# Kernel tuning notes

Measured on AMD Instinct MI355X. Metric: run time of the kernel, lower is better.

The kernel has to match this reference:

```python
import jax, jax.numpy as jnp
import numpy as np

B, S, H, NH, FF, L = 2, 2048, 768, 12, 3072, 2
DH = H // NH
EPS = 1e-12
NEG = -10000.0


def setup_inputs() -> dict:
    key = jax.random.key(0)
    ks = jax.random.split(key, 10)
    w = lambda k, shp: jax.random.normal(k, shp, dtype=jnp.float32) * 0.02
    return {
        'hidden_states': jax.random.normal(ks[0], (B, S, H), dtype=jnp.float32),
        'attention_mask': jnp.ones((B, S), jnp.float32),
        'bias_matrix': jax.random.normal(ks[1], (S, S), dtype=jnp.float32) * 0.1,
        'bias_coef': jnp.ones((), jnp.float32),
        'Wq': w(ks[2], (L, H, H)), 'bq': jnp.zeros((L, H), jnp.float32),
        'Wk': w(ks[3], (L, H, H)), 'bk': jnp.zeros((L, H), jnp.float32),
        'Wv': w(ks[4], (L, H, H)), 'bv': jnp.zeros((L, H), jnp.float32),
        'Wo': w(ks[5], (L, H, H)), 'bo': jnp.zeros((L, H), jnp.float32),
        'ln1_g': jnp.ones((L, H), jnp.float32), 'ln1_b': jnp.zeros((L, H), jnp.float32),
        'Wi': w(ks[6], (L, H, FF)), 'bi': jnp.zeros((L, FF), jnp.float32),
        'Wo2': w(ks[7], (L, FF, H)), 'bo2': jnp.zeros((L, H), jnp.float32),
        'ln2_g': jnp.ones((L, H), jnp.float32), 'ln2_b': jnp.zeros((L, H), jnp.float32),
    }


def _layer_norm(x, g, b):
    mu = jnp.mean(x, axis=-1, keepdims=True)
    var = jnp.mean(jnp.square(x - mu), axis=-1, keepdims=True)
    return (x - mu) * jax.lax.rsqrt(var + EPS) * g + b


def reference(hidden_states, attention_mask, bias_matrix, bias_coef,
              Wq, bq, Wk, bk, Wv, bv, Wo, bo, ln1_g, ln1_b,
              Wi, bi, Wo2, bo2, ln2_g, ln2_b):
    # extended additive mask: [B,1,1,S]
    ext_mask = (1.0 - attention_mask)[:, None, None, :] * NEG
    bias = bias_matrix[None, None] * bias_coef  # [1,1,S,S]
    x = hidden_states
    scale = 1.0 / np.sqrt(DH)
    for i in range(L):
        q = (x @ Wq[i] + bq[i]).reshape(B, S, NH, DH).transpose(0, 2, 1, 3)
        k = (x @ Wk[i] + bk[i]).reshape(B, S, NH, DH).transpose(0, 2, 1, 3)
        v = (x @ Wv[i] + bv[i]).reshape(B, S, NH, DH).transpose(0, 2, 1, 3)
        scores = jnp.einsum('bhqd,bhkd->bhqk', q, k) * scale
        scores = scores + bias + ext_mask
        probs = jax.nn.softmax(scores, axis=-1)  # dropout = identity (eval)
        ctx = jnp.einsum('bhqk,bhkd->bhqd', probs, v)
        ctx = ctx.transpose(0, 2, 1, 3).reshape(B, S, H)
        attn_out = ctx @ Wo[i] + bo[i]
        x = _layer_norm(attn_out + x, ln1_g[i], ln1_b[i])
        inter = jax.nn.gelu(x @ Wi[i] + bi[i], approximate=False)
        ffn_out = inter @ Wo2[i] + bo2[i]
        x = _layer_norm(ffn_out + x, ln2_g[i], ln2_b[i])
    return x
```

## Files before the change

kernel.cpp:

```cpp
#include <hip/hip_runtime.h>
#include <hip/hip_bf16.h>
#include <math.h>

#define BB     2
#define SS     2048
#define HH     768
#define NHEAD  12
#define DHEAD  64
#define FFD    3072
#define NLAYER 2
#define MTOK   (BB*SS)

typedef __attribute__((ext_vector_type(8))) short bf16x8;
typedef __attribute__((ext_vector_type(4))) short bf16x4;
typedef __attribute__((ext_vector_type(4))) float f32x4;

__device__ __forceinline__ short f2bs(float f) {
    union { float f; unsigned u; } v; v.f = f;
    unsigned r = v.u + 0x7FFF + ((v.u >> 16) & 1);
    return (short)(r >> 16);
}
__device__ __forceinline__ float bs2f(short s) {
    union { unsigned u; float f; } v; v.u = ((unsigned)(unsigned short)s) << 16;
    return v.f;
}
__device__ __forceinline__ void gl2lds16(const short* g, short* l) {
    __builtin_amdgcn_global_load_lds(
        (const __attribute__((address_space(1))) unsigned int*)g,
        (__attribute__((address_space(3))) unsigned int*)l, 16, 0, 0);
}

struct TJobs { const float* src[8]; short* dst[8]; };

__global__ __launch_bounds__(256)
void transpose_cvt_batch(TJobs jobs, int K, int N)
{
    const float* __restrict__ W  = jobs.src[blockIdx.z];
    short* __restrict__ Wt = jobs.dst[blockIdx.z];
    __shared__ short tile[32][33];
    const int k0 = blockIdx.x * 32, n0 = blockIdx.y * 32;
    const int tx = threadIdx.x & 31, ty = threadIdx.x >> 5;
#pragma unroll
    for (int i = 0; i < 4; i++)
        tile[ty + i*8][tx] = f2bs(W[(size_t)(k0 + ty + i*8) * N + n0 + tx]);
    __syncthreads();
#pragma unroll
    for (int i = 0; i < 4; i++)
        Wt[(size_t)(n0 + ty + i*8) * K + k0 + tx] = tile[tx][ty + i*8];
}

__global__ __launch_bounds__(256)
void cvt_bf16(const float* __restrict__ src, short* __restrict__ dst, int n)
{
    const int i = blockIdx.x * 256 + threadIdx.x;
    if (i < n) dst[i] = f2bs(src[i]);
}

__global__ __launch_bounds__(256)
void pack_bias(const float* __restrict__ bq, const float* __restrict__ bk,
               const float* __restrict__ bv, float* __restrict__ bqkv)
{
    const int t = blockIdx.x * 256 + threadIdx.x;
    if (t >= NLAYER * 2304) return;
    const int l = t / 2304, r = t % 2304;
    const float* src = (r < 768) ? bq : (r < 1536 ? bk : bv);
    bqkv[t] = src[l*768 + (r % 768)];
}

__global__ __launch_bounds__(256)
void bias_frag_prep(const float* __restrict__ biasM, const float* __restrict__ mask,
                    const float* __restrict__ coefp, short* __restrict__ bFrag)
{
    __shared__ float tile[64][129];
    const int tid = threadIdx.x;
    const int qb = blockIdx.x, q0 = qb*64, k0 = blockIdx.y*128;
#pragma unroll
    for (int p = 0; p < 8; p++) {
        const int row = p*8 + (tid >> 5);
        const int col = (tid & 31) * 4;
        float4 v = *(const float4*)&biasM[(size_t)(q0 + row)*SS + k0 + col];
        tile[row][col+0] = v.x; tile[row][col+1] = v.y;
        tile[row][col+2] = v.z; tile[row][col+3] = v.w;
    }
    __syncthreads();
    const float coef = coefp[0];
    const int lane = tid & 63, w = tid >> 6;
    const int l16 = lane & 15, g = lane >> 4;
    const int qrow = w*16 + l16;
#pragma unroll
    for (int b = 0; b < BB; b++) {
#pragma unroll
        for (int kt = 0; kt < 8; kt++) {
            bf16x4 o;
#pragma unroll
            for (int r = 0; r < 4; r++) {
                const int kk = kt*16 + g*4 + r;
                const float madd = (1.f - mask[b*SS + k0 + kk]) * (-10000.0f);
                o[r] = f2bs(tile[qrow][kk] * coef + madd);
            }
            const size_t idx = ((((size_t)b*32 + qb)*4 + w)*128 + (k0>>4) + kt)*256 + lane*4;
            *(bf16x4*)&bFrag[idx] = o;
        }
    }
}

__global__ __launch_bounds__(256)
void gemm_mfma(const short* __restrict__ A, const short* __restrict__ Bt,
               const float* __restrict__ bias, short* __restrict__ C, int ldc,
               int M, int N, int K, int gelu, short* __restrict__ VtOut, int vsplit)
{
    __shared__ short sA[2][128*32];
    __shared__ short sB[2][128*32];
    const int tid  = threadIdx.x;
    const int w    = tid >> 6;
    const int lane = tid & 63;
    const int l16  = lane & 15, g = lane >> 4;
    const int wm   = w & 1, wn = w >> 1;
    const size_t m0 = (size_t)blockIdx.y * 128, n0 = (size_t)blockIdx.x * 128;

    const int srow = lane >> 2;
    const int kc   = lane & 3;

    f32x4 acc[4][4];
#pragma unroll
    for (int i = 0; i < 4; i++)
#pragma unroll
        for (int j = 0; j < 4; j++) acc[i][j] = (f32x4){0.f,0.f,0.f,0.f};

    const short* gA0 = A  + (m0 + w*32 +      srow) * (size_t)K + kc*8;
    const short* gA1 = A  + (m0 + w*32 + 16 + srow) * (size_t)K + kc*8;
    const short* gB0 = Bt + (n0 + w*32 +      srow) * (size_t)K + kc*8;
    const short* gB1 = Bt + (n0 + w*32 + 16 + srow) * (size_t)K + kc*8;
    const int oA0 = (w*32     )*32, oA1 = (w*32 + 16)*32;

    for (int k0 = 0; k0 < K; k0 += 64) {
        gl2lds16(gA0 + k0,      &sA[0][oA0]);
        gl2lds16(gA1 + k0,      &sA[0][oA1]);
        gl2lds16(gB0 + k0,      &sB[0][oA0]);
        gl2lds16(gB1 + k0,      &sB[0][oA1]);
        gl2lds16(gA0 + k0 + 32, &sA[1][oA0]);
        gl2lds16(gA1 + k0 + 32, &sA[1][oA1]);
        gl2lds16(gB0 + k0 + 32, &sB[1][oA0]);
        gl2lds16(gB1 + k0 + 32, &sB[1][oA1]);
        __syncthreads();

#pragma unroll
        for (int s = 0; s < 2; s++) {
            bf16x8 af[4], bfr[4];
#pragma unroll
            for (int mt = 0; mt < 4; mt++)
                af[mt] = *(const bf16x8*)&sA[s][(wm*64 + mt*16 + l16)*32 + g*8];
#pragma unroll
            for (int nt = 0; nt < 4; nt++)
                bfr[nt] = *(const bf16x8*)&sB[s][(wn*64 + nt*16 + l16)*32 + g*8];
#pragma unroll
            for (int mt = 0; mt < 4; mt++)
#pragma unroll
                for (int nt = 0; nt < 4; nt++)
                    acc[mt][nt] = __builtin_amdgcn_mfma_f32_16x16x32_bf16(
                                      af[mt], bfr[nt], acc[mt][nt], 0, 0, 0);
        }
        __syncthreads();
    }

#pragma unroll
    for (int mt = 0; mt < 4; mt++) {
        const size_t row0 = m0 + wm*64 + mt*16 + g*4;
#pragma unroll
        for (int nt = 0; nt < 4; nt++) {
            const size_t col = n0 + wn*64 + nt*16 + l16;
            if ((int)col >= vsplit) {
                short4 t;
                t.x = f2bs(acc[mt][nt][0] + bias[col]);
                t.y = f2bs(acc[mt][nt][1] + bias[col]);
                t.z = f2bs(acc[mt][nt][2] + bias[col]);
                t.w = f2bs(acc[mt][nt][3] + bias[col]);
                *(short4*)&VtOut[(size_t)(col - vsplit)*MTOK + row0] = t;
            } else {
#pragma unroll
                for (int r = 0; r < 4; r++) {
                    float v = acc[mt][nt][r] + bias[col];
                    if (gelu) v = 0.5f * v * (1.f + erff(v * 0.70710678118f));
                    C[(row0 + r) * (size_t)ldc + col] = f2bs(v);
                }
            }
        }
    }
}

__global__ __launch_bounds__(256)
void gemm_mfma_n64(const short* __restrict__ A, const short* __restrict__ Bt,
                   const float* __restrict__ bias, short* __restrict__ C, int ldc,
                   int M, int N, int K, int gelu)
{
    __shared__ short sA[2][128*32];
    __shared__ short sB[2][64*32];
    const int tid  = threadIdx.x;
    const int w    = tid >> 6;
    const int lane = tid & 63;
    const int l16  = lane & 15, g = lane >> 4;
    const int wm   = w & 1, wn = w >> 1;
    const size_t m0 = (size_t)blockIdx.y * 128, n0 = (size_t)blockIdx.x * 64;

    const int srow = lane >> 2;
    const int kc   = lane & 3;

    f32x4 acc[4][2];
#pragma unroll
    for (int i = 0; i < 4; i++)
#pragma unroll
        for (int j = 0; j < 2; j++) acc[i][j] = (f32x4){0.f,0.f,0.f,0.f};

    const short* gA0 = A  + (m0 + w*32 +      srow) * (size_t)K + kc*8;
    const short* gA1 = A  + (m0 + w*32 + 16 + srow) * (size_t)K + kc*8;
    const short* gB0 = Bt + (n0 + w*16 +      srow) * (size_t)K + kc*8;
    const int oA0 = (w*32     )*32, oA1 = (w*32 + 16)*32, oB0 = (w*16)*32;

    for (int k0 = 0; k0 < K; k0 += 64) {
        gl2lds16(gA0 + k0,      &sA[0][oA0]);
        gl2lds16(gA1 + k0,      &sA[0][oA1]);
        gl2lds16(gB0 + k0,      &sB[0][oB0]);
        gl2lds16(gA0 + k0 + 32, &sA[1][oA0]);
        gl2lds16(gA1 + k0 + 32, &sA[1][oA1]);
        gl2lds16(gB0 + k0 + 32, &sB[1][oB0]);
        __syncthreads();

#pragma unroll
        for (int s = 0; s < 2; s++) {
            bf16x8 af[4], bfr[2];
#pragma unroll
            for (int mt = 0; mt < 4; mt++)
                af[mt] = *(const bf16x8*)&sA[s][(wm*64 + mt*16 + l16)*32 + g*8];
#pragma unroll
            for (int nt = 0; nt < 2; nt++)
                bfr[nt] = *(const bf16x8*)&sB[s][(wn*32 + nt*16 + l16)*32 + g*8];
#pragma unroll
            for (int mt = 0; mt < 4; mt++)
#pragma unroll
                for (int nt = 0; nt < 2; nt++)
                    acc[mt][nt] = __builtin_amdgcn_mfma_f32_16x16x32_bf16(
                                      af[mt], bfr[nt], acc[mt][nt], 0, 0, 0);
        }
        __syncthreads();
    }

#pragma unroll
    for (int mt = 0; mt < 4; mt++) {
        const size_t row0 = m0 + wm*64 + mt*16 + g*4;
#pragma unroll
        for (int nt = 0; nt < 2; nt++) {
            const size_t col = n0 + wn*32 + nt*16 + l16;
#pragma unroll
            for (int r = 0; r < 4; r++) {
                float v = acc[mt][nt][r] + bias[col];
                if (gelu) v = 0.5f * v * (1.f + erff(v * 0.70710678118f));
                C[(row0 + r) * (size_t)ldc + col] = f2bs(v);
            }
        }
    }
}

__global__ __launch_bounds__(256, 4)
void attn_fused(const short* __restrict__ QK, const short* __restrict__ Vt,
                const short* __restrict__ bFrag, short* __restrict__ CTX)
{
    __shared__ short sK[128*72];
    __shared__ short sV[64*136];

    const int qb  = blockIdx.x;
    const int q0  = qb * 64;
    const int h   = blockIdx.y;
    const int b   = blockIdx.z;
    const int tid = threadIdx.x;
    const int w   = tid >> 6;
    const int lane = tid & 63;
    const int l16 = lane & 15;
    const int g   = lane >> 4;
    const float scale = 0.125f;

    const short* qrow = QK + ((size_t)(b*SS) + q0 + w*16 + l16) * 1536 + h*64;
    bf16x8 bQ0 = *(const bf16x8*)(qrow + g*8);
    bf16x8 bQ1 = *(const bf16x8*)(qrow + 32 + g*8);

    f32x4 O[4];
#pragma unroll
    for (int d = 0; d < 4; d++) O[d] = (f32x4){0.f,0.f,0.f,0.f};
    float m_q = -1e30f, l_q = 0.f;

    const int krow = tid >> 3, kch = tid & 7;
    const int vrow = tid >> 4, vch = tid & 15;
    const short* Kg = QK + ((size_t)(b*SS) + krow)*1536 + 768 + h*64 + kch*8;
    const short* Vg = Vt + ((size_t)(h*64 + vrow))*MTOK + b*SS + vch*8;
    const short* bF = bFrag + ((((size_t)b*32 + qb)*4 + w)*128)*256 + lane*4;

    bf16x8 kreg[4], vreg[4];
#pragma unroll
    for (int p = 0; p < 4; p++) {
        kreg[p] = *(const bf16x8*)(Kg + (size_t)(p*32)*1536);
        vreg[p] = *(const bf16x8*)(Vg + (size_t)(p*16)*MTOK);
    }

    for (int k0 = 0; k0 < SS; k0 += 128) {
        const short* bFt = bF + ((size_t)(k0 >> 4))*256;
        bf16x4 bb[8];
#pragma unroll
        for (int t = 0; t < 8; t++)
            bb[t] = *(const bf16x4*)(bFt + (size_t)t*256);

#pragma unroll
        for (int p = 0; p < 4; p++) {
            *(bf16x8*)&sK[(p*32 + krow)*72 + kch*8]   = kreg[p];
            *(bf16x8*)&sV[(p*16 + vrow)*136 + vch*8]  = vreg[p];
        }
        __syncthreads();

        if (k0 + 128 < SS) {
#pragma unroll
            for (int p = 0; p < 4; p++) {
                kreg[p] = *(const bf16x8*)(Kg + (size_t)(k0 + 128 + p*32)*1536);
                vreg[p] = *(const bf16x8*)(Vg + (size_t)(p*16)*MTOK + k0 + 128);
            }
        }

        float S[8][4];
#pragma unroll
        for (int t = 0; t < 8; t++) {
            bf16x8 aK0 = *(const bf16x8*)&sK[(t*16 + l16)*72 + g*8];
            bf16x8 aK1 = *(const bf16x8*)&sK[(t*16 + l16)*72 + 32 + g*8];
            f32x4 c = (f32x4){0.f,0.f,0.f,0.f};
            c = __builtin_amdgcn_mfma_f32_16x16x32_bf16(aK0, bQ0, c, 0, 0, 0);
            c = __builtin_amdgcn_mfma_f32_16x16x32_bf16(aK1, bQ1, c, 0, 0, 0);
#pragma unroll
            for (int r = 0; r < 4; r++)
                S[t][r] = c[r]*scale + bs2f(bb[t][r]);
        }

        float tm[8];
#pragma unroll
        for (int t = 0; t < 8; t++)
            tm[t] = fmaxf(fmaxf(S[t][0], S[t][1]), fmaxf(S[t][2], S[t][3]));
        float mx = fmaxf(fmaxf(fmaxf(tm[0], tm[1]), fmaxf(tm[2], tm[3])),
                         fmaxf(fmaxf(tm[4], tm[5]), fmaxf(tm[6], tm[7])));
        mx = fmaxf(mx, __shfl_xor(mx, 16));
        mx = fmaxf(mx, __shfl_xor(mx, 32));
        const float mnew  = fmaxf(m_q, mx);
        const float alpha = __expf(m_q - mnew);
        float ts[8];
#pragma unroll
        for (int t = 0; t < 8; t++) {
            float p0 = __expf(S[t][0] - mnew);
            float p1 = __expf(S[t][1] - mnew);
            float p2 = __expf(S[t][2] - mnew);
            float p3 = __expf(S[t][3] - mnew);
            S[t][0] = p0; S[t][1] = p1; S[t][2] = p2; S[t][3] = p3;
            ts[t] = (p0 + p1) + (p2 + p3);
        }
        float rs = ((ts[0] + ts[1]) + (ts[2] + ts[3]))
                 + ((ts[4] + ts[5]) + (ts[6] + ts[7]));
        rs += __shfl_xor(rs, 16);
        rs += __shfl_xor(rs, 32);
        l_q = l_q * alpha + rs;
        m_q = mnew;

#pragma unroll
        for (int r = 0; r < 4; r++) {
            const float ar = __shfl(alpha, g*4 + r);
#pragma unroll
            for (int d = 0; d < 4; d++) O[d][r] *= ar;
        }

#define PVU(u)                                                                 \
        {                                                                      \
            unsigned pa, pb, pc, pe;                                           \
            asm("v_cvt_pk_bf16_f32 %0, %1, %2" : "=v"(pa)                      \
                : "v"(S[2*(u)][0]),   "v"(S[2*(u)][1]));                       \
            asm("v_cvt_pk_bf16_f32 %0, %1, %2" : "=v"(pb)                      \
                : "v"(S[2*(u)][2]),   "v"(S[2*(u)][3]));                       \
            asm("v_cvt_pk_bf16_f32 %0, %1, %2" : "=v"(pc)                      \
                : "v"(S[2*(u)+1][0]), "v"(S[2*(u)+1][1]));                     \
            asm("v_cvt_pk_bf16_f32 %0, %1, %2" : "=v"(pe)                      \
                : "v"(S[2*(u)+1][2]), "v"(S[2*(u)+1][3]));                     \
            asm("v_permlane32_swap_b32 %0, %1" : "+v"(pa), "+v"(pc));          \
            asm("v_permlane16_swap_b32 %0, %1" : "+v"(pa), "+v"(pc));          \
            asm("v_permlane32_swap_b32 %0, %1" : "+v"(pb), "+v"(pe));          \
            asm("v_permlane16_swap_b32 %0, %1" : "+v"(pb), "+v"(pe));          \
            union { unsigned uw[4]; bf16x8 v; } P_;                            \
            P_.uw[0] = pa; P_.uw[1] = pb; P_.uw[2] = pc; P_.uw[3] = pe;        \
            _Pragma("unroll")                                                  \
            for (int d = 0; d < 4; d++) {                                      \
                bf16x8 vv = *(const bf16x8*)&sV[(d*16 + l16)*136 + (u)*32 + g*8]; \
                O[d] = __builtin_amdgcn_mfma_f32_16x16x32_bf16(                \
                           P_.v, vv, O[d], 0, 0, 0);                           \
            }                                                                  \
        }
        PVU(0)
        PVU(1)
        PVU(2)
        PVU(3)
#undef PVU

        __syncthreads();
    }

    float linv[4];
#pragma unroll
    for (int r = 0; r < 4; r++)
        linv[r] = 1.f / __shfl(l_q, g*4 + r);
#pragma unroll
    for (int d = 0; d < 4; d++)
#pragma unroll
        for (int r = 0; r < 4; r++)
            CTX[((size_t)(b*SS) + q0 + w*16 + g*4 + r)*HH + h*64 + d*16 + l16]
                = f2bs(O[d][r] * linv[r]);
}

__global__ __launch_bounds__(256)
void add_ln(const short* __restrict__ A, const short* __restrict__ R,
            const float* __restrict__ g, const float* __restrict__ beta,
            short* __restrict__ Out, float* __restrict__ OutF)
{
    const int lane = threadIdx.x & 63;
    const int row  = blockIdx.x * 4 + (threadIdx.x >> 6);
    const size_t base = (size_t)row * HH;

    float v[12];
    float s = 0.f;
#pragma unroll
    for (int p = 0; p < 3; p++) {
        const int c = p*256 + lane*4;
        bf16x4 av = *(const bf16x4*)&A[base + c];
        bf16x4 rv = *(const bf16x4*)&R[base + c];
#pragma unroll
        for (int j = 0; j < 4; j++) {
            float x = bs2f(av[j]) + bs2f(rv[j]);
            v[p*4 + j] = x;
            s += x;
        }
    }
    s += __shfl_xor(s, 1);  s += __shfl_xor(s, 2);  s += __shfl_xor(s, 4);
    s += __shfl_xor(s, 8);  s += __shfl_xor(s, 16); s += __shfl_xor(s, 32);
    const float mu = s * (1.f / HH);

    float s2 = 0.f;
#pragma unroll
    for (int j = 0; j < 12; j++) { float d = v[j] - mu; s2 += d * d; }
    s2 += __shfl_xor(s2, 1);  s2 += __shfl_xor(s2, 2);  s2 += __shfl_xor(s2, 4);
    s2 += __shfl_xor(s2, 8);  s2 += __shfl_xor(s2, 16); s2 += __shfl_xor(s2, 32);
    const float rstd = rsqrtf(s2 * (1.f / HH) + 1e-12f);

#pragma unroll
    for (int p = 0; p < 3; p++) {
        const int c = p*256 + lane*4;
        float4 gv = *(const float4*)&g[c];
        float4 bv = *(const float4*)&beta[c];
        float o0 = (v[p*4+0] - mu) * rstd * gv.x + bv.x;
        float o1 = (v[p*4+1] - mu) * rstd * gv.y + bv.y;
        float o2 = (v[p*4+2] - mu) * rstd * gv.z + bv.z;
        float o3 = (v[p*4+3] - mu) * rstd * gv.w + bv.w;
        bf16x4 ov; ov[0] = f2bs(o0); ov[1] = f2bs(o1); ov[2] = f2bs(o2); ov[3] = f2bs(o3);
        *(bf16x4*)&Out[base + c] = ov;
        if (OutF) {
            float4 of; of.x = o0; of.y = o1; of.z = o2; of.w = o3;
            *(float4*)&OutF[base + c] = of;
        }
    }
}

extern "C" void kernel_launch(void* const* d_in, const int* in_sizes, int n_in,
                              void* d_out, int out_size, void* d_ws, size_t ws_size,
                              hipStream_t stream)
{
    const float* hs    = (const float*)d_in[0];
    const float* mask  = (const float*)d_in[1];
    const float* biasM = (const float*)d_in[2];
    const float* coef  = (const float*)d_in[3];
    const float* Wq    = (const float*)d_in[4];
    const float* bq    = (const float*)d_in[5];
    const float* Wk    = (const float*)d_in[6];
    const float* bk    = (const float*)d_in[7];
    const float* Wv    = (const float*)d_in[8];
    const float* bv    = (const float*)d_in[9];
    const float* Wo    = (const float*)d_in[10];
    const float* bo    = (const float*)d_in[11];
    const float* ln1g  = (const float*)d_in[12];
    const float* ln1b  = (const float*)d_in[13];
    const float* Wi    = (const float*)d_in[14];
    const float* bi    = (const float*)d_in[15];
    const float* Wo2   = (const float*)d_in[16];
    const float* bo2   = (const float*)d_in[17];
    const float* ln2g  = (const float*)d_in[18];
    const float* ln2b  = (const float*)d_in[19];

    const size_t sH   = (size_t)MTOK * HH;
    const size_t sQK  = (size_t)MTOK * 1536;
    const size_t sVt  = (size_t)HH * MTOK;
    const size_t WPL  = 7077888;
    short* wt    = (short*)d_ws;
    float* bqkv  = (float*)(wt + 2*WPL);
    short* bFrag = (short*)(bqkv + 2*2304);
    short* X     = bFrag + (size_t)2*SS*SS;
    short* X2    = X  + sH;
    short* QK    = X2 + sH;
    short* Vt    = QK + sQK;
    short* CTX   = Vt + sVt;
    short* TMP   = QK;
    short* INTER = QK;
    short* TMP2  = X;

    const dim3 blk(256);

    TJobs jH, jI, jO;
    for (int l = 0; l < NLAYER; l++) {
        short* wl = wt + (size_t)l * WPL;
        jH.src[l*4+0] = Wq + (size_t)l*HH*HH;  jH.dst[l*4+0] = wl;
        jH.src[l*4+1] = Wk + (size_t)l*HH*HH;  jH.dst[l*4+1] = wl + 768*768;
        jH.src[l*4+2] = Wv + (size_t)l*HH*HH;  jH.dst[l*4+2] = wl + 1536*768;
        jH.src[l*4+3] = Wo + (size_t)l*HH*HH;  jH.dst[l*4+3] = wl + 1769472;
        jI.src[l] = Wi  + (size_t)l*HH*FFD;    jI.dst[l] = wl + 2359296;
        jO.src[l] = Wo2 + (size_t)l*FFD*HH;    jO.dst[l] = wl + 4718592;
    }
    transpose_cvt_batch<<<dim3(24,24,8), blk, 0, stream>>>(jH, HH, HH);
    transpose_cvt_batch<<<dim3(24,96,2), blk, 0, stream>>>(jI, HH, FFD);
    transpose_cvt_batch<<<dim3(96,24,2), blk, 0, stream>>>(jO, FFD, HH);
    bias_frag_prep<<<dim3(SS/64, SS/128), blk, 0, stream>>>(biasM, mask, coef, bFrag);
    pack_bias<<<dim3((NLAYER*2304 + 255)/256), blk, 0, stream>>>(bq, bk, bv, bqkv);
    cvt_bf16<<<dim3((int)((sH + 255)/256)), blk, 0, stream>>>(hs, X, (int)sH);

    const dim3 gQKV(2304/128, MTOK/128);
    const dim3 gH64(HH/64,    MTOK/128);
    const dim3 gFF (FFD/128,  MTOK/128);
    const dim3 gA  (SS/64, NHEAD, BB);
    const dim3 gLN (MTOK/4);
    const int NOSPLIT = 1 << 30;

    for (int l = 0; l < NLAYER; l++) {
        short* wl = wt + (size_t)l * WPL;
        gemm_mfma<<<gQKV, blk, 0, stream>>>(X, wl, bqkv + l*2304, QK, 1536,
                                            MTOK, 2304, HH, 0, Vt, 1536);
        attn_fused<<<gA, blk, 0, stream>>>(QK, Vt, bFrag, CTX);
        gemm_mfma_n64<<<gH64, blk, 0, stream>>>(CTX, wl + 1769472, bo + l*HH, TMP, HH,
                                                MTOK, HH, HH, 0);
        add_ln<<<gLN, blk, 0, stream>>>(TMP, X, ln1g + l*HH, ln1b + l*HH, X2, nullptr);
        gemm_mfma<<<gFF, blk, 0, stream>>>(X2, wl + 2359296, bi + l*FFD, INTER, FFD,
                                           MTOK, FFD, HH, 1, nullptr, NOSPLIT);
        gemm_mfma_n64<<<gH64, blk, 0, stream>>>(INTER, wl + 4718592, bo2 + l*HH, TMP2, HH,
                                                MTOK, HH, FFD, 0);
        add_ln<<<gLN, blk, 0, stream>>>(TMP2, X2, ln2g + l*HH, ln2b + l*HH, X,
                                        (l == NLAYER-1) ? (float*)d_out : nullptr);
    }
}
```

Before: 573.5 us.

## Split-K the N=768 GEMMs with fp32 partials reduced in LayerNorm; fold softmax scale

The two N=768 output GEMMs now split K in half across gridDim.z and write fp32 partial sums. The add+LayerNorm kernel sums the two partials, adds the bias and the residual, which doubles the number of blocks for those under-filled GEMMs. Separately, the 1/sqrt(d)*log2e factor is folded into the Q projection epilogue and the additive bias tile is pre-scaled by log2e, so attention uses exp2f and drops a multiply per score. Attention launch bounds drop from 4 to 3 waves per SIMD. The cost is extra fp32 partial traffic (two 4096x768 fp32 buffers) written and read back per GEMM.

```diff
diff --git a/kernel.cpp b/kernel.cpp
--- a/kernel.cpp
+++ b/kernel.cpp
@@ -10,6 +10,8 @@
 #define FFD    3072
 #define NLAYER 2
 #define MTOK   (BB*SS)
+#define LOG2E  1.4426950408889634f
+#define QSCALE 0.18033688011112042f
 
 typedef __attribute__((ext_vector_type(8))) short bf16x8;
 typedef __attribute__((ext_vector_type(4))) short bf16x4;
@@ -96,7 +98,7 @@
             for (int r = 0; r < 4; r++) {
                 const int kk = kt*16 + g*4 + r;
                 const float madd = (1.f - mask[b*SS + k0 + kk]) * (-10000.0f);
-                o[r] = f2bs(tile[qrow][kk] * coef + madd);
+                o[r] = f2bs((tile[qrow][kk] * coef + madd) * LOG2E);
             }
             const size_t idx = ((((size_t)b*32 + qb)*4 + w)*128 + (k0>>4) + kt)*256 + lane*4;
             *(bf16x4*)&bFrag[idx] = o;
@@ -107,7 +109,8 @@
 __global__ __launch_bounds__(256)
 void gemm_mfma(const short* __restrict__ A, const short* __restrict__ Bt,
                const float* __restrict__ bias, short* __restrict__ C, int ldc,
-               int M, int N, int K, int gelu, short* __restrict__ VtOut, int vsplit)
+               int M, int N, int K, int gelu, short* __restrict__ VtOut, int vsplit,
+               float qscale, int qcols)
 {
     __shared__ short sA[2][128*32];
     __shared__ short sB[2][128*32];
@@ -180,6 +183,7 @@
 #pragma unroll
                 for (int r = 0; r < 4; r++) {
                     float v = acc[mt][nt][r] + bias[col];
+                    if ((int)col < qcols) v *= qscale;
                     if (gelu) v = 0.5f * v * (1.f + erff(v * 0.70710678118f));
                     C[(row0 + r) * (size_t)ldc + col] = f2bs(v);
                 }
@@ -189,10 +193,11 @@
 }
 
 __global__ __launch_bounds__(256)
-void gemm_mfma_n64(const short* __restrict__ A, const short* __restrict__ Bt,
-                   const float* __restrict__ bias, short* __restrict__ C, int ldc,
-                   int M, int N, int K, int gelu)
-{
+void gemm_n64_splitk(const short* __restrict__ A, const short* __restrict__ Bt,
+                     float* __restrict__ P, int K)
+{
+    const int K2 = K >> 1;
+    const int z  = blockIdx.z;
     __shared__ short sA[2][128*32];
     __shared__ short sB[2][64*32];
     const int tid  = threadIdx.x;
@@ -211,12 +216,12 @@
 #pragma unroll
         for (int j = 0; j < 2; j++) acc[i][j] = (f32x4){0.f,0.f,0.f,0.f};
 
-    const short* gA0 = A  + (m0 + w*32 +      srow) * (size_t)K + kc*8;
-    const short* gA1 = A  + (m0 + w*32 + 16 + srow) * (size_t)K + kc*8;
-    const short* gB0 = Bt + (n0 + w*16 +      srow) * (size_t)K + kc*8;
+    const short* gA0 = A  + (m0 + w*32 +      srow) * (size_t)K + z*K2 + kc*8;
+    const short* gA1 = A  + (m0 + w*32 + 16 + srow) * (size_t)K + z*K2 + kc*8;
+    const short* gB0 = Bt + (n0 + w*16 +      srow) * (size_t)K + z*K2 + kc*8;
     const int oA0 = (w*32     )*32, oA1 = (w*32 + 16)*32, oB0 = (w*16)*32;
 
-    for (int k0 = 0; k0 < K; k0 += 64) {
+    for (int k0 = 0; k0 < K2; k0 += 64) {
         gl2lds16(gA0 + k0,      &sA[0][oA0]);
         gl2lds16(gA1 + k0,      &sA[0][oA1]);
         gl2lds16(gB0 + k0,      &sB[0][oB0]);
@@ -244,6 +249,7 @@
         __syncthreads();
     }
 
+    float* Pz = P + (size_t)z * MTOK * HH;
 #pragma unroll
     for (int mt = 0; mt < 4; mt++) {
         const size_t row0 = m0 + wm*64 + mt*16 + g*4;
@@ -251,16 +257,13 @@
         for (int nt = 0; nt < 2; nt++) {
             const size_t col = n0 + wn*32 + nt*16 + l16;
 #pragma unroll
-            for (int r = 0; r < 4; r++) {
-                float v = acc[mt][nt][r] + bias[col];
-                if (gelu) v = 0.5f * v * (1.f + erff(v * 0.70710678118f));
-                C[(row0 + r) * (size_t)ldc + col] = f2bs(v);
-            }
-        }
-    }
-}
-
-__global__ __launch_bounds__(256, 4)
+            for (int r = 0; r < 4; r++)
+                Pz[(row0 + r) * (size_t)HH + col] = acc[mt][nt][r];
+        }
+    }
+}
+
+__global__ __launch_bounds__(256, 3)
 void attn_fused(const short* __restrict__ QK, const short* __restrict__ Vt,
                 const short* __restrict__ bFrag, short* __restrict__ CTX)
 {
@@ -276,7 +279,6 @@
     const int lane = tid & 63;
     const int l16 = lane & 15;
     const int g   = lane >> 4;
-    const float scale = 0.125f;
 
     const short* qrow = QK + ((size_t)(b*SS) + q0 + w*16 + l16) * 1536 + h*64;
     bf16x8 bQ0 = *(const bf16x8*)(qrow + g*8);
@@ -332,7 +334,7 @@
             c = __builtin_amdgcn_mfma_f32_16x16x32_bf16(aK1, bQ1, c, 0, 0, 0);
 #pragma unroll
             for (int r = 0; r < 4; r++)
-                S[t][r] = c[r]*scale + bs2f(bb[t][r]);
+                S[t][r] = c[r] + bs2f(bb[t][r]);
         }
 
         float tm[8];
@@ -344,14 +346,14 @@
         mx = fmaxf(mx, __shfl_xor(mx, 16));
         mx = fmaxf(mx, __shfl_xor(mx, 32));
         const float mnew  = fmaxf(m_q, mx);
-        const float alpha = __expf(m_q - mnew);
+        const float alpha = exp2f(m_q - mnew);
         float ts[8];
 #pragma unroll
         for (int t = 0; t < 8; t++) {
-            float p0 = __expf(S[t][0] - mnew);
-            float p1 = __expf(S[t][1] - mnew);
-            float p2 = __expf(S[t][2] - mnew);
-            float p3 = __expf(S[t][3] - mnew);
+            float p0 = exp2f(S[t][0] - mnew);
+            float p1 = exp2f(S[t][1] - mnew);
+            float p2 = exp2f(S[t][2] - mnew);
+            float p3 = exp2f(S[t][3] - mnew);
             S[t][0] = p0; S[t][1] = p1; S[t][2] = p2; S[t][3] = p3;
             ts[t] = (p0 + p1) + (p2 + p3);
         }
@@ -415,27 +417,31 @@
 }
 
 __global__ __launch_bounds__(256)
-void add_ln(const short* __restrict__ A, const short* __restrict__ R,
-            const float* __restrict__ g, const float* __restrict__ beta,
-            short* __restrict__ Out, float* __restrict__ OutF)
+void add_ln3(const float* __restrict__ P, const float* __restrict__ bvec,
+             const short* __restrict__ R,
+             const float* __restrict__ g, const float* __restrict__ beta,
+             short* __restrict__ Out, float* __restrict__ OutF)
 {
     const int lane = threadIdx.x & 63;
     const int row  = blockIdx.x * 4 + (threadIdx.x >> 6);
     const size_t base = (size_t)row * HH;
+    const size_t sH = (size_t)MTOK * HH;
 
     float v[12];
     float s = 0.f;
 #pragma unroll
     for (int p = 0; p < 3; p++) {
         const int c = p*256 + lane*4;
-        bf16x4 av = *(const bf16x4*)&A[base + c];
+        float4 p0 = *(const float4*)&P[base + c];
+        float4 p1 = *(const float4*)&P[sH + base + c];
+        float4 bv4 = *(const float4*)&bvec[c];
         bf16x4 rv = *(const bf16x4*)&R[base + c];
-#pragma unroll
-        for (int j = 0; j < 4; j++) {
-            float x = bs2f(av[j]) + bs2f(rv[j]);
-            v[p*4 + j] = x;
-            s += x;
-        }
+        float x0 = p0.x + p1.x + bv4.x + bs2f(rv[0]);
+        float x1 = p0.y + p1.y + bv4.y + bs2f(rv[1]);
+        float x2 = p0.z + p1.z + bv4.z + bs2f(rv[2]);
+        float x3 = p0.w + p1.w + bv4.w + bs2f(rv[3]);
+        v[p*4+0] = x0; v[p*4+1] = x1; v[p*4+2] = x2; v[p*4+3] = x3;
+        s += (x0 + x1) + (x2 + x3);
     }
     s += __shfl_xor(s, 1);  s += __shfl_xor(s, 2);  s += __shfl_xor(s, 4);
     s += __shfl_xor(s, 8);  s += __shfl_xor(s, 16); s += __shfl_xor(s, 32);
@@ -503,9 +509,8 @@
     short* QK    = X2 + sH;
     short* Vt    = QK + sQK;
     short* CTX   = Vt + sVt;
-    short* TMP   = QK;
+    float* PK    = (float*)(CTX + sH);
     short* INTER = QK;
-    short* TMP2  = X;
 
     const dim3 blk(256);
 
@@ -527,7 +532,7 @@
     cvt_bf16<<<dim3((int)((sH + 255)/256)), blk, 0, stream>>>(hs, X, (int)sH);
 
     const dim3 gQKV(2304/128, MTOK/128);
-    const dim3 gH64(HH/64,    MTOK/128);
+    const dim3 gSK (HH/64,    MTOK/128, 2);
     const dim3 gFF (FFD/128,  MTOK/128);
     const dim3 gA  (SS/64, NHEAD, BB);
     const dim3 gLN (MTOK/4);
@@ -536,16 +541,17 @@
     for (int l = 0; l < NLAYER; l++) {
         short* wl = wt + (size_t)l * WPL;
         gemm_mfma<<<gQKV, blk, 0, stream>>>(X, wl, bqkv + l*2304, QK, 1536,
-                                            MTOK, 2304, HH, 0, Vt, 1536);
+                                            MTOK, 2304, HH, 0, Vt, 1536,
+                                            QSCALE, 768);
         attn_fused<<<gA, blk, 0, stream>>>(QK, Vt, bFrag, CTX);
-        gemm_mfma_n64<<<gH64, blk, 0, stream>>>(CTX, wl + 1769472, bo + l*HH, TMP, HH,
-                                                MTOK, HH, HH, 0);
-        add_ln<<<gLN, blk, 0, stream>>>(TMP, X, ln1g + l*HH, ln1b + l*HH, X2, nullptr);
+        gemm_n64_splitk<<<gSK, blk, 0, stream>>>(CTX, wl + 1769472, PK, HH);
+        add_ln3<<<gLN, blk, 0, stream>>>(PK, bo + l*HH, X, ln1g + l*HH, ln1b + l*HH,
+                                         X2, nullptr);
         gemm_mfma<<<gFF, blk, 0, stream>>>(X2, wl + 2359296, bi + l*FFD, INTER, FFD,
-                                           MTOK, FFD, HH, 1, nullptr, NOSPLIT);
-        gemm_mfma_n64<<<gH64, blk, 0, stream>>>(INTER, wl + 4718592, bo2 + l*HH, TMP2, HH,
-                                                MTOK, HH, FFD, 0);
-        add_ln<<<gLN, blk, 0, stream>>>(TMP2, X2, ln2g + l*HH, ln2b + l*HH, X,
-                                        (l == NLAYER-1) ? (float*)d_out : nullptr);
-    }
-}
+                                           MTOK, FFD, HH, 1, nullptr, NOSPLIT,
+                                           1.f, 0);
+        gemm_n64_splitk<<<gSK, blk, 0, stream>>>(INTER, wl + 4718592, PK, FFD);
+        add_ln3<<<gLN, blk, 0, stream>>>(PK, bo2 + l*HH, X2, ln2g + l*HH, ln2b + l*HH,
+                                         X, (l == NLAYER-1) ? (float*)d_out : nullptr);
+    }
+}
```

Result: no change. 569.8 us (-0.6%).
